# Kernel tuning notes

Hardware: AMD Instinct MI355X
Metric: run time of the kernel (lower is better)

## Reference

```python
import jax, jax.numpy as jnp
import numpy as np

N_MOL = 48; N_PER = 80; N = N_MOL * N_PER          # 3840 atoms
F = 128; K = 64; B = 5; NRI = 2; NRA = 2; NRO = 1   # PhysNet defaults
SR_CUT = 10.0
KEHALF = 7.199822675975274
LN2 = 0.6931471805599453


def ssp(x):  # shifted softplus
    return jax.nn.softplus(x) - LN2


def _res(x, W, b):  # pre-activation residual: x + Dense(act(Dense(act(x))))
    h = ssp(x)
    h = ssp(h @ W[0] + b[0])
    return x + h @ W[1] + b[1]


def _energy(Ra, emb, rbf_centers, rbf_widths, Wrbf, Wi, bi, Wj, bj,
            resI_W, resI_b, Wd, bd, u, resA_W, resA_b, resO_W, resO_b,
            Wout, bout, Escale, Eshift, Qscale, Qshift,
            Za, idx_i, idx_j, batch_seg):
    # interatomic distances on edge list
    Dij = jnp.sqrt(jax.nn.relu(jnp.sum((Ra[idx_i] - Ra[idx_j]) ** 2, -1)))  # [E]
    # RBF layer with smooth cutoff: phi(r)*exp(-w*(exp(-r)-c)^2)
    xr = Dij / SR_CUT
    cut = jnp.where(Dij < SR_CUT, 1 - 6 * xr**5 + 15 * xr**4 - 10 * xr**3, 0.0)
    rbf = cut[:, None] * jnp.exp(-rbf_widths * (jnp.exp(-Dij)[:, None] - rbf_centers) ** 2)  # [E,K]

    x = emb[Za]  # [N,F]
    Ea = jnp.zeros((N,), x.dtype)
    Qa = jnp.zeros((N,), x.dtype)
    for blk in range(B):
        # interaction layer: gather over idx_j, rbf-gated message, scatter to idx_i
        g = rbf @ Wrbf[blk]                     # [E,F]
        xa = ssp(x)
        mi = ssp(xa @ Wi[blk] + bi[blk])        # [N,F]
        mj = ssp(xa @ Wj[blk] + bj[blk])        # [N,F]
        m = mi + jax.ops.segment_sum(g * mj[idx_j], idx_i, num_segments=N)
        for r in range(NRI):
            m = _res(m, resI_W[blk, r], resI_b[blk, r])
        m = ssp(m)
        x = u[blk] * x + m @ Wd[blk] + bd[blk]
        for r in range(NRA):
            x = _res(x, resA_W[blk, r], resA_b[blk, r])
        # output block
        o = x
        for r in range(NRO):
            o = _res(o, resO_W[blk, r], resO_b[blk, r])
        o = ssp(o) @ Wout[blk] + bout[blk]      # [N,2]
        Ea = Ea + o[:, 0]
        Qa = Qa + o[:, 1]
    Ea = Escale[Za] * Ea + Eshift[Za] + 0.0 * jnp.sum(Ra, -1)
    Qa = Qscale[Za] * Qa + Qshift[Za]
    # charge conservation scaling (Q_tot = 0)
    Na = jax.ops.segment_sum(jnp.ones_like(Qa), batch_seg, num_segments=N_MOL)
    Qa = Qa + ((-jax.ops.segment_sum(Qa, batch_seg, num_segments=N_MOL)) / Na)[batch_seg]
    # shielded electrostatics (lr_cut=None branch)
    DijS = jnp.sqrt(Dij * Dij + 1.0)
    c = SR_CUT / 2
    xs = Dij / c
    sw = jnp.where(Dij < c, 6 * xs**5 - 15 * xs**4 + 10 * xs**3, 1.0)
    Eele = KEHALF * Qa[idx_i] * Qa[idx_j] * ((1.0 - sw) / DijS + sw / Dij)
    Ea = Ea + jax.ops.segment_sum(Eele, idx_i, num_segments=N)
    return jax.ops.segment_sum(Ea, batch_seg, num_segments=N_MOL)  # [N_MOL]


def setup_inputs() -> dict:
    rng = np.random.default_rng(0)
    Za = jnp.asarray(rng.integers(1, 95, size=N), dtype=jnp.int32)
    Ra = jnp.asarray(rng.uniform(0.0, 8.0, size=(N, 3)), dtype=jnp.float32)
    # all ordered intra-molecule pairs (i != j), as PhysNet's batch_collate_fn builds
    ii, jj = np.meshgrid(np.arange(N_PER), np.arange(N_PER), indexing='ij')
    msk = ii != jj
    ii = ii[msk]; jj = jj[msk]
    base = (np.arange(N_MOL) * N_PER)[:, None]
    idx_i = jnp.asarray((ii[None, :] + base).reshape(-1), dtype=jnp.int32)
    idx_j = jnp.asarray((jj[None, :] + base).reshape(-1), dtype=jnp.int32)
    batch_seg = jnp.asarray(np.repeat(np.arange(N_MOL), N_PER), dtype=jnp.int32)
    k = jax.random.split(jax.random.key(0), 16)
    s = 1.0 / np.sqrt(F)
    nrm = lambda kk, shape, scale: jax.random.normal(kk, shape, jnp.float32) * scale
    width = float(((2.0 / K) * (1.0 - np.exp(-SR_CUT))) ** -2)
    return dict(
        Za=Za, Ra=Ra, idx_i=idx_i, idx_j=idx_j, batch_seg=batch_seg,
        emb=nrm(k[0], (95, F), 1.0),
        rbf_centers=jnp.linspace(np.exp(-SR_CUT), 1.0, K, dtype=jnp.float32),
        rbf_widths=jnp.full((K,), width, jnp.float32),
        Wrbf=nrm(k[1], (B, K, F), 1.0 / np.sqrt(K)),
        Wi=nrm(k[2], (B, F, F), s), bi=jnp.zeros((B, F), jnp.float32),
        Wj=nrm(k[3], (B, F, F), s), bj=jnp.zeros((B, F), jnp.float32),
        resI_W=nrm(k[4], (B, NRI, 2, F, F), s), resI_b=jnp.zeros((B, NRI, 2, F), jnp.float32),
        Wd=nrm(k[5], (B, F, F), s), bd=jnp.zeros((B, F), jnp.float32),
        u=jnp.ones((B, F), jnp.float32),
        resA_W=nrm(k[6], (B, NRA, 2, F, F), s), resA_b=jnp.zeros((B, NRA, 2, F), jnp.float32),
        resO_W=nrm(k[7], (B, NRO, 2, F, F), s), resO_b=jnp.zeros((B, NRO, 2, F), jnp.float32),
        Wout=nrm(k[8], (B, F, 2), 0.01), bout=jnp.zeros((B, 2), jnp.float32),
        Escale=jnp.ones((95,), jnp.float32), Eshift=jnp.zeros((95,), jnp.float32),
        Qscale=jnp.ones((95,), jnp.float32), Qshift=jnp.zeros((95,), jnp.float32),
    )


def reference(Za, Ra, idx_i, idx_j, batch_seg, emb, rbf_centers, rbf_widths,
              Wrbf, Wi, bi, Wj, bj, resI_W, resI_b, Wd, bd, u,
              resA_W, resA_b, resO_W, resO_b, Wout, bout,
              Escale, Eshift, Qscale, Qshift):
    return _energy(Ra, emb, rbf_centers, rbf_widths, Wrbf, Wi, bi, Wj, bj,
                   resI_W, resI_b, Wd, bd, u, resA_W, resA_b, resO_W, resO_b,
                   Wout, bout, Escale, Eshift, Qscale, Qshift,
                   Za, idx_i, idx_j, batch_seg)
```

## Files before the change

kernel.cpp:

```cpp
#include <hip/hip_runtime.h>

#define NATOM 3840
#define NMOL 48
#define NPER 80
#define FD 128
#define KR 64
#define NBLOCK 5

constexpr float SR_CUT_C = 10.0f;
constexpr float KEHALF_C = 7.199822675975274f;
constexpr float LN2_C    = 0.6931471805599453f;

using bf16x8 = __attribute__((ext_vector_type(8))) short;
using f32x4  = __attribute__((ext_vector_type(4))) float;

__device__ __forceinline__ float sspf(float x) {
    return fmaxf(x, 0.0f) + __logf(1.0f + __expf(-fabsf(x))) - LN2_C;
}

__device__ __forceinline__ void split2(float v, short& hi, short& lo) {
    unsigned u = __float_as_uint(v);
    hi = (short)(u >> 16);
    float l = v - __uint_as_float(u & 0xFFFF0000u);
    lo = (short)(__float_as_uint(l) >> 16);
}

__device__ __forceinline__ void mj_store(short* mjTg, int gr, int f, float v) {
    int mol = gr / NPER;
    int jl  = gr - mol * NPER;
    short hi, lo; split2(v, hi, lo);
    size_t mo = (size_t)mol * 24576;
    int off = (jl >> 5) * 4096 + f * 32 + ((jl >> 3) & 3) * 8 + (jl & 7);
    mjTg[mo + off] = hi;
    mjTg[mo + 12288 + off] = lo;
}

__device__ __forceinline__ int plane_idx(int r, int f) {
    int s = f >> 3;
    int sp = (s & 8) | ((s ^ (r & 7)) & 7);
    return r * 128 + sp * 8 + (f & 7);
}

__device__ __forceinline__ void plane_store(short* Ahi, short* Alo, int r, int f, float v) {
    int idx = plane_idx(r, f);
    short hi, lo; split2(v, hi, lo);
    Ahi[idx] = hi; Alo[idx] = lo;
}

__device__ __forceinline__ void stage_w_wave(short* dstBase, const short* srcBase, int w, int lane) {
#pragma unroll
    for (int it = 0; it < 16; ++it) {
        int boff = w * 16384 + it * 1024;
        __builtin_amdgcn_global_load_lds(
            (const __attribute__((address_space(1))) unsigned int*)((const char*)srcBase + boff + lane * 16),
            (__attribute__((address_space(3))) unsigned int*)((char*)dstBase + boff),
            16, 0, 0);
    }
}

__device__ __forceinline__ void gemm_core(const short* Ahi, const short* Alo,
    const short* Wl, int lane, int fq0, f32x4 acc[2])
{
    const int r = lane & 15, h = lane >> 4;
    bf16x8 afh[4], afl[4];
#pragma unroll
    for (int kt = 0; kt < 4; ++kt) {
        int s = kt * 4 + h;
        int sp = (s & 8) | ((s ^ (r & 7)) & 7);
        afh[kt] = *(const bf16x8*)&Ahi[r * 128 + sp * 8];
        afl[kt] = *(const bf16x8*)&Alo[r * 128 + sp * 8];
    }
#pragma unroll
    for (int ft = 0; ft < 2; ++ft) {
        f32x4 a = {0.f, 0.f, 0.f, 0.f};
#pragma unroll
        for (int kt = 0; kt < 4; ++kt) {
            const short* bp = &Wl[((fq0 + ft) * 4 + kt) * 1024 + lane * 8];
            bf16x8 bh = *(const bf16x8*)bp;
            bf16x8 bl = *(const bf16x8*)(bp + 512);
            a = __builtin_amdgcn_mfma_f32_16x16x32_bf16(afh[kt], bl, a, 0, 0, 0);
            a = __builtin_amdgcn_mfma_f32_16x16x32_bf16(afl[kt], bh, a, 0, 0, 0);
            a = __builtin_amdgcn_mfma_f32_16x16x32_bf16(afh[kt], bh, a, 0, 0, 0);
        }
        acc[ft] = a;
    }
}

__global__ __launch_bounds__(256) void k_prep(
    const float* __restrict__ Wi, const float* __restrict__ Wj,
    const float* __restrict__ rIW, const float* __restrict__ Wd,
    const float* __restrict__ rAW, const float* __restrict__ rOW,
    short* __restrict__ prepW)
{
    const int m = blockIdx.x, tid = threadIdx.x;
    const float* src;
    if (m == 65) src = Wi;
    else if (m == 66) src = Wj;
    else {
        int bb = m / 13, slot = m % 13;
        switch (slot) {
            case 0: case 1: case 2: case 3:
                src = rIW + (size_t)((bb * 2 + (slot >> 1)) * 2 + (slot & 1)) * 16384; break;
            case 4: src = Wd + (size_t)bb * 16384; break;
            case 5: case 6: case 7: case 8: {
                int ss = slot - 5;
                src = rAW + (size_t)((bb * 2 + (ss >> 1)) * 2 + (ss & 1)) * 16384; break;
            }
            case 9:  src = Wi + (size_t)((bb + 1 < 5) ? (bb + 1) : 0) * 16384; break;
            case 10: src = Wj + (size_t)((bb + 1 < 5) ? (bb + 1) : 0) * 16384; break;
            default: src = rOW + (size_t)(bb * 2 + (slot - 11)) * 16384; break;
        }
    }
    short* dst = prepW + (size_t)m * 32768;
#pragma unroll
    for (int i = 0; i < 8; ++i) {
        int tr = tid + i * 256;
        int ft = tr >> 8, kt = (tr >> 6) & 3, l = tr & 63;
        int f = ft * 16 + (l & 15);
        int k0 = kt * 32 + (l >> 4) * 8;
        bf16x8 hi8, lo8;
#pragma unroll
        for (int e = 0; e < 8; ++e) {
            float v = src[(size_t)(k0 + e) * FD + f];
            short hh, ll; split2(v, hh, ll);
            hi8[e] = hh; lo8[e] = ll;
        }
        size_t o = (size_t)(ft * 4 + kt) * 1024 + (size_t)l * 8;
        *(bf16x8*)&dst[o] = hi8;
        *(bf16x8*)&dst[o + 512] = lo8;
    }
}

__global__ __launch_bounds__(256) void k_first(
    const int* __restrict__ Za, const float* __restrict__ emb,
    const short* __restrict__ Wprep,
    const float* __restrict__ bi, const float* __restrict__ bj,
    float* __restrict__ X, float* __restrict__ MI, short* __restrict__ mjTg,
    float* __restrict__ Ea, float* __restrict__ Qa)
{
    __shared__ short Ahi[2048], Alo[2048];
    __shared__ short Wl[2][32768];
    const int tid = threadIdx.x, lane = tid & 63, w = tid >> 6;
    const int row0 = blockIdx.x * 16;
    const int fq0 = w * 2;
    const int col0 = w * 32 + (lane & 15), col1 = col0 + 16;
    const int hh = lane >> 4;

    stage_w_wave(Wl[0], Wprep + (size_t)65 * 32768, w, lane);

    for (int idx = tid; idx < 2048; idx += 256) {
        int rr = idx >> 7, f = idx & 127;
        float v = emb[(size_t)Za[row0 + rr] * FD + f];
        X[(size_t)(row0 + rr) * FD + f] = v;
        plane_store(Ahi, Alo, rr, f, sspf(v));
    }
    if (tid < 16) { Ea[row0 + tid] = 0.f; Qa[row0 + tid] = 0.f; }
    if ((row0 % NPER) == 0) {
        short* mb = mjTg + (size_t)(row0 / NPER) * 24576;
        for (int idx = tid; idx < 2048; idx += 256) {
            int f = idx >> 4, t = idx & 15;
            mb[8192 + f * 32 + 16 + t] = 0;
            mb[12288 + 8192 + f * 32 + 16 + t] = 0;
        }
    }
    __syncthreads();

    stage_w_wave(Wl[1], Wprep + (size_t)66 * 32768, w, lane);

    f32x4 acc[2];
    gemm_core(Ahi, Alo, Wl[0], lane, fq0, acc);
    {
        float b0 = bi[col0], b1 = bi[col1];
#pragma unroll
        for (int reg = 0; reg < 4; ++reg) {
            int rw = hh * 4 + reg;
            MI[(size_t)(row0 + rw) * FD + col0] = sspf(acc[0][reg] + b0);
            MI[(size_t)(row0 + rw) * FD + col1] = sspf(acc[1][reg] + b1);
        }
    }
    asm volatile("s_waitcnt vmcnt(0)" ::: "memory");
    gemm_core(Ahi, Alo, Wl[1], lane, fq0, acc);
    {
        float b0 = bj[col0], b1 = bj[col1];
#pragma unroll
        for (int reg = 0; reg < 4; ++reg) {
            int gr = row0 + hh * 4 + reg;
            mj_store(mjTg, gr, col0, sspf(acc[0][reg] + b0));
            mj_store(mjTg, gr, col1, sspf(acc[1][reg] + b1));
        }
    }
}

__global__ __launch_bounds__(256) void k_tail(
    const float* __restrict__ M, float* __restrict__ X,
    const short* __restrict__ Wprep, int b,
    const float* __restrict__ rIb, const float* __restrict__ bd,
    const float* __restrict__ u, const float* __restrict__ rAb,
    const float* __restrict__ bi, const float* __restrict__ bj,
    const float* __restrict__ rOb, const float* __restrict__ Wout,
    const float* __restrict__ bout,
    float* __restrict__ MI, short* __restrict__ mjTg,
    float* __restrict__ Ea, float* __restrict__ Qa)
{
    __shared__ short Ahi[2048], Alo[2048];
    __shared__ short Wl[2][32768];
    __shared__ float eq[16][5][2];

    const int tid = threadIdx.x, lane = tid & 63, w = tid >> 6;
    const int row0 = blockIdx.x * 16;
    const int NG = (b < 4) ? 13 : 11;
    const int fq0 = w * 2;
    const int col0 = w * 32 + (lane & 15), col1 = col0 + 16;
    const int hh = lane >> 4;

    auto lgOf = [&](int gg) { return (b < 4 || gg < 9) ? gg : gg + 2; };

    stage_w_wave(Wl[0], Wprep + (size_t)(b * 13 + lgOf(0)) * 32768, w, lane);

    float vreg[2][4], xreg[2][4];
#pragma unroll
    for (int reg = 0; reg < 4; ++reg) {
        int rw = hh * 4 + reg;
        vreg[0][reg] = M[(size_t)(row0 + rw) * FD + col0];
        vreg[1][reg] = M[(size_t)(row0 + rw) * FD + col1];
        xreg[0][reg] = X[(size_t)(row0 + rw) * FD + col0];
        xreg[1][reg] = X[(size_t)(row0 + rw) * FD + col1];
    }
    for (int idx = tid; idx < 2048; idx += 256) {
        int rr = idx >> 7, f = idx & 127;
        plane_store(Ahi, Alo, rr, f, sspf(M[(size_t)(row0 + rr) * FD + f]));
    }
    __syncthreads();

    f32x4 acc[2];
    for (int g = 0; g < NG; ++g) {
        const int cur = g & 1;
        if (g > 0) {
            asm volatile("s_waitcnt lgkmcnt(0)\n\ts_barrier" ::: "memory");
            asm volatile("s_waitcnt vmcnt(0)" ::: "memory");
        }
        if (g + 1 < NG)
            stage_w_wave(Wl[cur ^ 1], Wprep + (size_t)(b * 13 + lgOf(g + 1)) * 32768, w, lane);

        int lg = lgOf(g);
        const float* bptr;
        switch (lg) {
            case 0:  bptr = rIb + ((size_t)(b * 2 + 0) * 2 + 0) * FD; break;
            case 1:  bptr = rIb + ((size_t)(b * 2 + 0) * 2 + 1) * FD; break;
            case 2:  bptr = rIb + ((size_t)(b * 2 + 1) * 2 + 0) * FD; break;
            case 3:  bptr = rIb + ((size_t)(b * 2 + 1) * 2 + 1) * FD; break;
            case 4:  bptr = bd + (size_t)b * FD; break;
            case 5:  bptr = rAb + ((size_t)(b * 2 + 0) * 2 + 0) * FD; break;
            case 6:  bptr = rAb + ((size_t)(b * 2 + 0) * 2 + 1) * FD; break;
            case 7:  bptr = rAb + ((size_t)(b * 2 + 1) * 2 + 0) * FD; break;
            case 8:  bptr = rAb + ((size_t)(b * 2 + 1) * 2 + 1) * FD; break;
            case 9:  bptr = bi + (size_t)(b + 1) * FD; break;
            case 10: bptr = bj + (size_t)(b + 1) * FD; break;
            case 11: bptr = rOb + (size_t)(b * 2 + 0) * FD; break;
            default: bptr = rOb + (size_t)(b * 2 + 1) * FD; break;
        }
        float bv0 = bptr[col0], bv1 = bptr[col1];
        float uv0 = 0.f, uv1 = 0.f;
        if (lg == 4) { uv0 = u[(size_t)b * FD + col0]; uv1 = u[(size_t)b * FD + col1]; }

        gemm_core(Ahi, Alo, Wl[cur], lane, fq0, acc);

        asm volatile("s_waitcnt lgkmcnt(0)\n\ts_barrier" ::: "memory");

        const bool isT = (lg == 0) | (lg == 2) | (lg == 5) | (lg == 7) | (lg == 11);
        const bool isV = (lg == 1) | (lg == 3) | (lg == 6) | (lg == 8) | (lg == 12);
        if (isT) {
#pragma unroll
            for (int reg = 0; reg < 4; ++reg) {
                int rw = hh * 4 + reg;
                plane_store(Ahi, Alo, rw, col0, sspf(acc[0][reg] + bv0));
                plane_store(Ahi, Alo, rw, col1, sspf(acc[1][reg] + bv1));
            }
        } else if (isV) {
#pragma unroll
            for (int reg = 0; reg < 4; ++reg) {
                int rw = hh * 4 + reg;
                float nv0 = acc[0][reg] + bv0 + vreg[0][reg];
                float nv1 = acc[1][reg] + bv1 + vreg[1][reg];
                vreg[0][reg] = nv0; vreg[1][reg] = nv1;
                if (lg != 12) {
                    plane_store(Ahi, Alo, rw, col0, sspf(nv0));
                    plane_store(Ahi, Alo, rw, col1, sspf(nv1));
                }
                if (lg == 8) {
                    X[(size_t)(row0 + rw) * FD + col0] = nv0;
                    X[(size_t)(row0 + rw) * FD + col1] = nv1;
                }
            }
        } else if (lg == 4) {
#pragma unroll
            for (int reg = 0; reg < 4; ++reg) {
                int rw = hh * 4 + reg;
                float nv0 = acc[0][reg] + bv0 + uv0 * xreg[0][reg];
                float nv1 = acc[1][reg] + bv1 + uv1 * xreg[1][reg];
                vreg[0][reg] = nv0; vreg[1][reg] = nv1;
                plane_store(Ahi, Alo, rw, col0, sspf(nv0));
                plane_store(Ahi, Alo, rw, col1, sspf(nv1));
            }
        } else if (lg == 9) {
#pragma unroll
            for (int reg = 0; reg < 4; ++reg) {
                int rw = hh * 4 + reg;
                MI[(size_t)(row0 + rw) * FD + col0] = sspf(acc[0][reg] + bv0);
                MI[(size_t)(row0 + rw) * FD + col1] = sspf(acc[1][reg] + bv1);
            }
        } else {
#pragma unroll
            for (int reg = 0; reg < 4; ++reg) {
                int gr = row0 + hh * 4 + reg;
                mj_store(mjTg, gr, col0, sspf(acc[0][reg] + bv0));
                mj_store(mjTg, gr, col1, sspf(acc[1][reg] + bv1));
            }
        }
    }
    float pe[4], pq[4];
#pragma unroll
    for (int reg = 0; reg < 4; ++reg) {
        float s0 = sspf(vreg[0][reg]), s1 = sspf(vreg[1][reg]);
        pe[reg] = s0 * Wout[col0 * 2 + 0] + s1 * Wout[col1 * 2 + 0];
        pq[reg] = s0 * Wout[col0 * 2 + 1] + s1 * Wout[col1 * 2 + 1];
#pragma unroll
        for (int mk = 1; mk < 16; mk <<= 1) {
            pe[reg] += __shfl_xor(pe[reg], mk);
            pq[reg] += __shfl_xor(pq[reg], mk);
        }
        if ((lane & 15) == 0) {
            eq[hh * 4 + reg][w][0] = pe[reg];
            eq[hh * 4 + reg][w][1] = pq[reg];
        }
    }
    __syncthreads();
    if (tid < 16) {
        float e = eq[tid][0][0] + eq[tid][1][0] + eq[tid][2][0] + eq[tid][3][0];
        float q = eq[tid][0][1] + eq[tid][1][1] + eq[tid][2][1] + eq[tid][3][1];
        Ea[row0 + tid] += e + bout[0];
        Qa[row0 + tid] += q + bout[1];
    }
}

__global__ __launch_bounds__(512, 2) void k_msg(
    const float* __restrict__ Ra, const float* __restrict__ MI,
    const short* __restrict__ mjTg, const float* __restrict__ centers,
    const float* __restrict__ widths, const float* __restrict__ Wrbf,
    float* __restrict__ MOUT)
{
    __shared__ short Bf[24576];
    __shared__ float Wt[8192];
    __shared__ float px[NPER], py[NPER], pz[NPER];

    const int tid  = threadIdx.x;
    const int lane = tid & 63;
    const int w    = tid >> 6;
    const int mol  = blockIdx.x / (NPER / 8);
    const int ig   = blockIdx.x % (NPER / 8);
    const int base = mol * NPER;
    const int i    = ig * 8 + w;

    const int col = lane & 15;
    const int grp = lane >> 4;

    {
        const char* src = (const char*)mjTg + (size_t)mol * 49152 + w * 6144 + lane * 16;
        char* dst = (char*)Bf + w * 6144;
#pragma unroll
        for (int it = 0; it < 6; ++it) {
            __builtin_amdgcn_global_load_lds(
                (const __attribute__((address_space(1))) unsigned int*)(src + it * 1024),
                (__attribute__((address_space(3))) unsigned int*)(dst + it * 1024),
                16, 0, 0);
        }
    }
    for (int idx = tid; idx < KR * FD; idx += 512) {
        int k = idx >> 7, f = idx & 127;
        Wt[(k >> 2) * 512 + f * 4 + (k & 3)] = Wrbf[idx];
    }
    if (tid < NPER) {
        px[tid] = Ra[(size_t)(base + tid) * 3 + 0];
        py[tid] = Ra[(size_t)(base + tid) * 3 + 1];
        pz[tid] = Ra[(size_t)(base + tid) * 3 + 2];
    }

    float cent[4], wid[4];
#pragma unroll
    for (int kt = 0; kt < 4; ++kt) {
        cent[kt] = centers[kt * 16 + col];
        wid[kt]  = widths[kt * 16 + col];
    }

    f32x4 acc[4][8];
#pragma unroll
    for (int kt = 0; kt < 4; ++kt)
#pragma unroll
        for (int ft = 0; ft < 8; ++ft)
            acc[kt][ft] = (f32x4){0.f, 0.f, 0.f, 0.f};

    __syncthreads();

    const float xi = px[i], yi = py[i], zi = pz[i];

    for (int ch = 0; ch < 3; ++ch) {
        bf16x8 Ahi[4], Alo[4];
#pragma unroll
        for (int e = 0; e < 8; ++e) {
            int jg = ch * 32 + grp * 8 + e;
            float ed = 0.f, cut = 0.f;
            if (jg < NPER) {
                float dx = px[jg] - xi, dy = py[jg] - yi, dz = pz[jg] - zi;
                float d = sqrtf(dx * dx + dy * dy + dz * dz);
                ed = __expf(-d);
                if (jg != i && d < SR_CUT_C) {
                    float xr = d * (1.0f / SR_CUT_C);
                    float xr2 = xr * xr, xr3 = xr2 * xr;
                    cut = 1.0f - xr3 * (6.0f * xr2 - 15.0f * xr + 10.0f);
                }
            }
#pragma unroll
            for (int kt = 0; kt < 4; ++kt) {
                float t = ed - cent[kt];
                float val = cut * __expf(-wid[kt] * t * t);
                unsigned uv = __float_as_uint(val);
                Ahi[kt][e] = (short)(uv >> 16);
                float lv = val - __uint_as_float(uv & 0xFFFF0000u);
                Alo[kt][e] = (short)(__float_as_uint(lv) >> 16);
            }
        }

        const int cb = ch * 4096 + col * 32 + grp * 8;
#pragma unroll
        for (int ft = 0; ft < 8; ++ft) {
            bf16x8 bhi = *(const bf16x8*)&Bf[cb + ft * 512];
            bf16x8 blo = *(const bf16x8*)&Bf[12288 + cb + ft * 512];
            __builtin_amdgcn_s_setprio(1);
#pragma unroll
            for (int kt = 0; kt < 4; ++kt) {
                acc[kt][ft] = __builtin_amdgcn_mfma_f32_16x16x32_bf16(Ahi[kt], bhi, acc[kt][ft], 0, 0, 0);
                acc[kt][ft] = __builtin_amdgcn_mfma_f32_16x16x32_bf16(Alo[kt], bhi, acc[kt][ft], 0, 0, 0);
                acc[kt][ft] = __builtin_amdgcn_mfma_f32_16x16x32_bf16(Ahi[kt], blo, acc[kt][ft], 0, 0, 0);
            }
            __builtin_amdgcn_s_setprio(0);
        }
    }

    float part[8];
#pragma unroll
    for (int ft = 0; ft < 8; ++ft) part[ft] = 0.f;
#pragma unroll
    for (int kt = 0; kt < 4; ++kt) {
        const float* wrow = &Wt[(kt * 4 + grp) * 512 + col * 4];
#pragma unroll
        for (int ft = 0; ft < 8; ++ft) {
            float4 w4 = *(const float4*)(wrow + ft * 64);
            part[ft] += acc[kt][ft].x * w4.x + acc[kt][ft].y * w4.y
                      + acc[kt][ft].z * w4.z + acc[kt][ft].w * w4.w;
        }
    }
#pragma unroll
    for (int ft = 0; ft < 8; ++ft) {
        part[ft] += __shfl_xor(part[ft], 16);
        part[ft] += __shfl_xor(part[ft], 32);
    }
    float p0 = (grp == 0) ? part[0] : (grp == 1) ? part[1] : (grp == 2) ? part[2] : part[3];
    float p1 = (grp == 0) ? part[4] : (grp == 1) ? part[5] : (grp == 2) ? part[6] : part[7];
    const size_t go = (size_t)(base + i) * FD;
    MOUT[go + lane]      = MI[go + lane] + p0;
    MOUT[go + 64 + lane] = MI[go + 64 + lane] + p1;
}

__global__ __launch_bounds__(256) void k_final(
    const int* __restrict__ Za, const float* __restrict__ Ra,
    const float* __restrict__ Escale, const float* __restrict__ Eshift,
    const float* __restrict__ Qscale, const float* __restrict__ Qshift,
    const float* __restrict__ Ea, const float* __restrict__ Qa,
    float* __restrict__ out)
{
    __shared__ float qs[NPER], es[NPER], px[NPER], py[NPER], pz[NPER];
    __shared__ float red[256];
    const int mol = blockIdx.x, t = threadIdx.x;
    float q = 0.f;
    if (t < NPER) {
        int a = mol * NPER + t;
        int z = Za[a];
        es[t] = Escale[z] * Ea[a] + Eshift[z];
        q = Qscale[z] * Qa[a] + Qshift[z];
        px[t] = Ra[(size_t)a * 3 + 0];
        py[t] = Ra[(size_t)a * 3 + 1];
        pz[t] = Ra[(size_t)a * 3 + 2];
    }
    red[t] = q;
    __syncthreads();
    for (int s = 128; s > 0; s >>= 1) {
        if (t < s) red[t] += red[t + s];
        __syncthreads();
    }
    float qavg = red[0] / (float)NPER;
    __syncthreads();
    if (t < NPER) qs[t] = q - qavg;
    red[t] = 0.f;
    __syncthreads();

    float local = 0.f;
    const float c = SR_CUT_C * 0.5f;
    for (int p = t; p < NPER * NPER; p += 256) {
        int i = p / NPER, j = p % NPER;
        if (i == j) continue;
        float dx = px[i] - px[j], dy = py[i] - py[j], dz = pz[i] - pz[j];
        float d2 = dx * dx + dy * dy + dz * dz;
        float d = sqrtf(d2);
        float dS = sqrtf(d2 + 1.0f);
        float sw;
        if (d < c) {
            float xs = d / c;
            float xs2 = xs * xs, xs3 = xs2 * xs;
            sw = xs3 * (6.0f * xs2 - 15.0f * xs + 10.0f);
        } else {
            sw = 1.0f;
        }
        local += KEHALF_C * qs[i] * qs[j] * ((1.0f - sw) / dS + sw / d);
    }
    for (int a = t; a < NPER; a += 256) local += es[a];
    red[t] = local;
    __syncthreads();
    for (int s = 128; s > 0; s >>= 1) {
        if (t < s) red[t] += red[t + s];
        __syncthreads();
    }
    if (t == 0) out[mol] = red[0];
}

extern "C" void kernel_launch(void* const* d_in, const int* in_sizes, int n_in,
                              void* d_out, int out_size, void* d_ws, size_t ws_size,
                              hipStream_t stream)
{
    (void)in_sizes; (void)n_in; (void)out_size; (void)ws_size;

    const int*   Za     = (const int*)d_in[0];
    const float* Ra     = (const float*)d_in[1];
    const float* emb    = (const float*)d_in[5];
    const float* rbfc   = (const float*)d_in[6];
    const float* rbfw   = (const float*)d_in[7];
    const float* Wrbf   = (const float*)d_in[8];
    const float* Wi     = (const float*)d_in[9];
    const float* bi     = (const float*)d_in[10];
    const float* Wj     = (const float*)d_in[11];
    const float* bj     = (const float*)d_in[12];
    const float* rIW    = (const float*)d_in[13];
    const float* rIb    = (const float*)d_in[14];
    const float* Wd     = (const float*)d_in[15];
    const float* bd     = (const float*)d_in[16];
    const float* u      = (const float*)d_in[17];
    const float* rAW    = (const float*)d_in[18];
    const float* rAb    = (const float*)d_in[19];
    const float* rOW    = (const float*)d_in[20];
    const float* rOb    = (const float*)d_in[21];
    const float* Wout   = (const float*)d_in[22];
    const float* bout   = (const float*)d_in[23];
    const float* Escale = (const float*)d_in[24];
    const float* Eshift = (const float*)d_in[25];
    const float* Qscale = (const float*)d_in[26];
    const float* Qshift = (const float*)d_in[27];
    float* outp = (float*)d_out;

    float* ws = (float*)d_ws;
    const size_t NF = (size_t)NATOM * FD;
    float* x  = ws;
    float* mi = ws + NF;
    float* m  = ws + 2 * NF;
    float* Ea = ws + 3 * NF;
    float* Qa = Ea + NATOM;
    short* prepW = (short*)(ws + 3 * NF + 2 * NATOM);
    short* mjTg  = prepW + (size_t)67 * 32768;

    k_prep<<<67, 256, 0, stream>>>(Wi, Wj, rIW, Wd, rAW, rOW, prepW);
    k_first<<<NATOM / 16, 256, 0, stream>>>(Za, emb, prepW, bi, bj, x, mi, mjTg, Ea, Qa);

    for (int b = 0; b < NBLOCK; ++b) {
        k_msg<<<NMOL * (NPER / 8), 512, 0, stream>>>(
            Ra, mi, mjTg, rbfc, rbfw, Wrbf + (size_t)b * KR * FD, m);
        k_tail<<<NATOM / 16, 256, 0, stream>>>(
            m, x, prepW, b, rIb, bd, u, rAb, bi, bj, rOb,
            Wout + (size_t)b * FD * 2, bout + b * 2, mi, mjTg, Ea, Qa);
    }

    k_final<<<NMOL, 256, 0, stream>>>(Za, Ra, Escale, Eshift, Qscale, Qshift, Ea, Qa, outp);
}
```

Baseline: 348.5 us.

## Split tail kernel across eight waves and skip negligible RBF exponentials

The tail kernel moves from four to eight waves per block, with each wave computing a single 16-column tile instead of two. Each wave now stages half as much weight data and holds fewer accumulators, which spreads the per-row MLP work over more waves. The message kernel also skips the exponential and bf16 hi/lo split for RBF terms whose exponent exceeds 20 across the whole wave, writing zeros instead. That threshold leaves out values below about e^-20, a slight approximation, and adds a wave vote and a branch in the inner loop.

```diff
diff --git a/kernel.cpp b/kernel.cpp
--- a/kernel.cpp
+++ b/kernel.cpp
@@ -58,6 +58,17 @@
     }
 }
 
+__device__ __forceinline__ void stage_w_wave8(short* dstBase, const short* srcBase, int w, int lane) {
+#pragma unroll
+    for (int it = 0; it < 8; ++it) {
+        int boff = w * 8192 + it * 1024;
+        __builtin_amdgcn_global_load_lds(
+            (const __attribute__((address_space(1))) unsigned int*)((const char*)srcBase + boff + lane * 16),
+            (__attribute__((address_space(3))) unsigned int*)((char*)dstBase + boff),
+            16, 0, 0);
+    }
+}
+
 __device__ __forceinline__ void gemm_core(const short* Ahi, const short* Alo,
     const short* Wl, int lane, int fq0, f32x4 acc[2])
 {
@@ -84,6 +95,31 @@
         }
         acc[ft] = a;
     }
+}
+
+__device__ __forceinline__ void gemm_core1(const short* Ahi, const short* Alo,
+    const short* Wl, int lane, int fq, f32x4& acc)
+{
+    const int r = lane & 15, h = lane >> 4;
+    bf16x8 afh[4], afl[4];
+#pragma unroll
+    for (int kt = 0; kt < 4; ++kt) {
+        int s = kt * 4 + h;
+        int sp = (s & 8) | ((s ^ (r & 7)) & 7);
+        afh[kt] = *(const bf16x8*)&Ahi[r * 128 + sp * 8];
+        afl[kt] = *(const bf16x8*)&Alo[r * 128 + sp * 8];
+    }
+    f32x4 a = {0.f, 0.f, 0.f, 0.f};
+#pragma unroll
+    for (int kt = 0; kt < 4; ++kt) {
+        const short* bp = &Wl[(fq * 4 + kt) * 1024 + lane * 8];
+        bf16x8 bh = *(const bf16x8*)bp;
+        bf16x8 bl = *(const bf16x8*)(bp + 512);
+        a = __builtin_amdgcn_mfma_f32_16x16x32_bf16(afh[kt], bl, a, 0, 0, 0);
+        a = __builtin_amdgcn_mfma_f32_16x16x32_bf16(afl[kt], bh, a, 0, 0, 0);
+        a = __builtin_amdgcn_mfma_f32_16x16x32_bf16(afh[kt], bh, a, 0, 0, 0);
+    }
+    acc = a;
 }
 
 __global__ __launch_bounds__(256) void k_prep(
@@ -191,7 +227,7 @@
     }
 }
 
-__global__ __launch_bounds__(256) void k_tail(
+__global__ __launch_bounds__(512) void k_tail(
     const float* __restrict__ M, float* __restrict__ X,
     const short* __restrict__ Wprep, int b,
     const float* __restrict__ rIb, const float* __restrict__ bd,
@@ -204,35 +240,33 @@
 {
     __shared__ short Ahi[2048], Alo[2048];
     __shared__ short Wl[2][32768];
-    __shared__ float eq[16][5][2];
+    __shared__ float eq[16][8][2];
 
     const int tid = threadIdx.x, lane = tid & 63, w = tid >> 6;
     const int row0 = blockIdx.x * 16;
     const int NG = (b < 4) ? 13 : 11;
-    const int fq0 = w * 2;
-    const int col0 = w * 32 + (lane & 15), col1 = col0 + 16;
+    const int fq = w;
+    const int col0 = w * 16 + (lane & 15);
     const int hh = lane >> 4;
 
     auto lgOf = [&](int gg) { return (b < 4 || gg < 9) ? gg : gg + 2; };
 
-    stage_w_wave(Wl[0], Wprep + (size_t)(b * 13 + lgOf(0)) * 32768, w, lane);
-
-    float vreg[2][4], xreg[2][4];
+    stage_w_wave8(Wl[0], Wprep + (size_t)(b * 13 + lgOf(0)) * 32768, w, lane);
+
+    float vreg[4], xreg[4];
 #pragma unroll
     for (int reg = 0; reg < 4; ++reg) {
         int rw = hh * 4 + reg;
-        vreg[0][reg] = M[(size_t)(row0 + rw) * FD + col0];
-        vreg[1][reg] = M[(size_t)(row0 + rw) * FD + col1];
-        xreg[0][reg] = X[(size_t)(row0 + rw) * FD + col0];
-        xreg[1][reg] = X[(size_t)(row0 + rw) * FD + col1];
-    }
-    for (int idx = tid; idx < 2048; idx += 256) {
+        vreg[reg] = M[(size_t)(row0 + rw) * FD + col0];
+        xreg[reg] = X[(size_t)(row0 + rw) * FD + col0];
+    }
+    for (int idx = tid; idx < 2048; idx += 512) {
         int rr = idx >> 7, f = idx & 127;
         plane_store(Ahi, Alo, rr, f, sspf(M[(size_t)(row0 + rr) * FD + f]));
     }
     __syncthreads();
 
-    f32x4 acc[2];
+    f32x4 acc;
     for (int g = 0; g < NG; ++g) {
         const int cur = g & 1;
         if (g > 0) {
@@ -240,7 +274,7 @@
             asm volatile("s_waitcnt vmcnt(0)" ::: "memory");
         }
         if (g + 1 < NG)
-            stage_w_wave(Wl[cur ^ 1], Wprep + (size_t)(b * 13 + lgOf(g + 1)) * 32768, w, lane);
+            stage_w_wave8(Wl[cur ^ 1], Wprep + (size_t)(b * 13 + lgOf(g + 1)) * 32768, w, lane);
 
         int lg = lgOf(g);
         const float* bptr;
@@ -259,11 +293,11 @@
             case 11: bptr = rOb + (size_t)(b * 2 + 0) * FD; break;
             default: bptr = rOb + (size_t)(b * 2 + 1) * FD; break;
         }
-        float bv0 = bptr[col0], bv1 = bptr[col1];
-        float uv0 = 0.f, uv1 = 0.f;
-        if (lg == 4) { uv0 = u[(size_t)b * FD + col0]; uv1 = u[(size_t)b * FD + col1]; }
-
-        gemm_core(Ahi, Alo, Wl[cur], lane, fq0, acc);
+        float bv0 = bptr[col0];
+        float uv0 = 0.f;
+        if (lg == 4) uv0 = u[(size_t)b * FD + col0];
+
+        gemm_core1(Ahi, Alo, Wl[cur], lane, fq, acc);
 
         asm volatile("s_waitcnt lgkmcnt(0)\n\ts_barrier" ::: "memory");
 
@@ -271,59 +305,40 @@
         const bool isV = (lg == 1) | (lg == 3) | (lg == 6) | (lg == 8) | (lg == 12);
         if (isT) {
 #pragma unroll
+            for (int reg = 0; reg < 4; ++reg)
+                plane_store(Ahi, Alo, hh * 4 + reg, col0, sspf(acc[reg] + bv0));
+        } else if (isV) {
+#pragma unroll
             for (int reg = 0; reg < 4; ++reg) {
                 int rw = hh * 4 + reg;
-                plane_store(Ahi, Alo, rw, col0, sspf(acc[0][reg] + bv0));
-                plane_store(Ahi, Alo, rw, col1, sspf(acc[1][reg] + bv1));
-            }
-        } else if (isV) {
-#pragma unroll
-            for (int reg = 0; reg < 4; ++reg) {
-                int rw = hh * 4 + reg;
-                float nv0 = acc[0][reg] + bv0 + vreg[0][reg];
-                float nv1 = acc[1][reg] + bv1 + vreg[1][reg];
-                vreg[0][reg] = nv0; vreg[1][reg] = nv1;
-                if (lg != 12) {
-                    plane_store(Ahi, Alo, rw, col0, sspf(nv0));
-                    plane_store(Ahi, Alo, rw, col1, sspf(nv1));
-                }
-                if (lg == 8) {
-                    X[(size_t)(row0 + rw) * FD + col0] = nv0;
-                    X[(size_t)(row0 + rw) * FD + col1] = nv1;
-                }
+                float nv0 = acc[reg] + bv0 + vreg[reg];
+                vreg[reg] = nv0;
+                if (lg != 12) plane_store(Ahi, Alo, rw, col0, sspf(nv0));
+                if (lg == 8)  X[(size_t)(row0 + rw) * FD + col0] = nv0;
             }
         } else if (lg == 4) {
 #pragma unroll
             for (int reg = 0; reg < 4; ++reg) {
-                int rw = hh * 4 + reg;
-                float nv0 = acc[0][reg] + bv0 + uv0 * xreg[0][reg];
-                float nv1 = acc[1][reg] + bv1 + uv1 * xreg[1][reg];
-                vreg[0][reg] = nv0; vreg[1][reg] = nv1;
-                plane_store(Ahi, Alo, rw, col0, sspf(nv0));
-                plane_store(Ahi, Alo, rw, col1, sspf(nv1));
+                float nv0 = acc[reg] + bv0 + uv0 * xreg[reg];
+                vreg[reg] = nv0;
+                plane_store(Ahi, Alo, hh * 4 + reg, col0, sspf(nv0));
             }
         } else if (lg == 9) {
 #pragma unroll
-            for (int reg = 0; reg < 4; ++reg) {
-                int rw = hh * 4 + reg;
-                MI[(size_t)(row0 + rw) * FD + col0] = sspf(acc[0][reg] + bv0);
-                MI[(size_t)(row0 + rw) * FD + col1] = sspf(acc[1][reg] + bv1);
-            }
+            for (int reg = 0; reg < 4; ++reg)
+                MI[(size_t)(row0 + hh * 4 + reg) * FD + col0] = sspf(acc[reg] + bv0);
         } else {
 #pragma unroll
-            for (int reg = 0; reg < 4; ++reg) {
-                int gr = row0 + hh * 4 + reg;
-                mj_store(mjTg, gr, col0, sspf(acc[0][reg] + bv0));
-                mj_store(mjTg, gr, col1, sspf(acc[1][reg] + bv1));
-            }
+            for (int reg = 0; reg < 4; ++reg)
+                mj_store(mjTg, row0 + hh * 4 + reg, col0, sspf(acc[reg] + bv0));
         }
     }
     float pe[4], pq[4];
 #pragma unroll
     for (int reg = 0; reg < 4; ++reg) {
-        float s0 = sspf(vreg[0][reg]), s1 = sspf(vreg[1][reg]);
-        pe[reg] = s0 * Wout[col0 * 2 + 0] + s1 * Wout[col1 * 2 + 0];
-        pq[reg] = s0 * Wout[col0 * 2 + 1] + s1 * Wout[col1 * 2 + 1];
+        float s0 = sspf(vreg[reg]);
+        pe[reg] = s0 * Wout[col0 * 2 + 0];
+        pq[reg] = s0 * Wout[col0 * 2 + 1];
 #pragma unroll
         for (int mk = 1; mk < 16; mk <<= 1) {
             pe[reg] += __shfl_xor(pe[reg], mk);
@@ -336,8 +351,9 @@
     }
     __syncthreads();
     if (tid < 16) {
-        float e = eq[tid][0][0] + eq[tid][1][0] + eq[tid][2][0] + eq[tid][3][0];
-        float q = eq[tid][0][1] + eq[tid][1][1] + eq[tid][2][1] + eq[tid][3][1];
+        float e = 0.f, q = 0.f;
+#pragma unroll
+        for (int ww = 0; ww < 8; ++ww) { e += eq[tid][ww][0]; q += eq[tid][ww][1]; }
         Ea[row0 + tid] += e + bout[0];
         Qa[row0 + tid] += q + bout[1];
     }
@@ -422,11 +438,17 @@
 #pragma unroll
             for (int kt = 0; kt < 4; ++kt) {
                 float t = ed - cent[kt];
-                float val = cut * __expf(-wid[kt] * t * t);
-                unsigned uv = __float_as_uint(val);
-                Ahi[kt][e] = (short)(uv >> 16);
-                float lv = val - __uint_as_float(uv & 0xFFFF0000u);
-                Alo[kt][e] = (short)(__float_as_uint(lv) >> 16);
+                float a2 = wid[kt] * t * t;
+                if (__any(a2 < 20.0f)) {
+                    float val = cut * __expf(-a2);
+                    unsigned uv = __float_as_uint(val);
+                    Ahi[kt][e] = (short)(uv >> 16);
+                    float lv = val - __uint_as_float(uv & 0xFFFF0000u);
+                    Alo[kt][e] = (short)(__float_as_uint(lv) >> 16);
+                } else {
+                    Ahi[kt][e] = 0;
+                    Alo[kt][e] = 0;
+                }
             }
         }
 
@@ -581,7 +603,7 @@
     for (int b = 0; b < NBLOCK; ++b) {
         k_msg<<<NMOL * (NPER / 8), 512, 0, stream>>>(
             Ra, mi, mjTg, rbfc, rbfw, Wrbf + (size_t)b * KR * FD, m);
-        k_tail<<<NATOM / 16, 256, 0, stream>>>(
+        k_tail<<<NATOM / 16, 512, 0, stream>>>(
             m, x, prepW, b, rIb, bd, u, rAb, bi, bj, rOb,
             Wout + (size_t)b * FD * 2, bout + b * 2, mi, mjTg, Ea, Qa);
     }
```

After: 342.8 us (median of 2 runs). About the same (-1.7%).
